# Kernel tuning notes

Measured on AMD Instinct MI355X. Metric: run time of the kernel, lower is better.

The kernel has to match this reference:

```python
import jax, jax.numpy as jnp
import numpy as np

MAX_DISP = 48
PATCH = 3
OFFSET = 0
PAD = PATCH // 2
EPS = 1e-3


def _unfold(x, P, pad):
    # x: [B,C,H,W] -> [B,C,K2,H,W], K2 enumerated row-major over the PxP window
    B, C, H, W = x.shape
    xp = jnp.pad(x, ((0, 0), (0, 0), (pad, pad), (pad, pad)))
    return jnp.stack([xp[:, :, i:i + H, j:j + W]
                      for i in range(P) for j in range(P)], axis=2)


def _normalize(x, axes):
    # torch F.normalize: x / clamp(||x||_2, min=eps)
    n = jnp.sqrt(jnp.sum(x * x, axis=axes, keepdims=True))
    return x / jnp.maximum(n, EPS)


def setup_inputs() -> dict:
    key = jax.random.key(0)
    k1, k2, k3 = jax.random.split(key, 3)
    shp = (2, 32, 128, 416)
    return {
        "xl": jax.random.normal(k1, shp, dtype=jnp.float32),
        "xm": jax.random.normal(k2, shp, dtype=jnp.float32),
        "xr": jax.random.normal(k3, shp, dtype=jnp.float32),
    }


def reference(xl, xm, xr):
    B, C, H, W = xl.shape
    K2 = PATCH * PATCH
    scale = (C * K2) ** 0.5

    pl = _normalize(_unfold(xl, PATCH, PAD), (1, 2))  # [B,C,K2,H,W]
    pr = _normalize(_unfold(xr, PATCH, PAD), (1, 2))
    fl = _normalize(xm, (1,))                          # [B,C,H,W]

    # fl is constant over the K2 axis, so sum patches over K2 once for sim_L/sim_R
    Sl = pl.sum(axis=2)  # [B,C,H,W]
    Sr = pr.sum(axis=2)

    cL, cR, cLR = [], [], []
    for d in range(OFFSET, OFFSET + MAX_DISP):
        if d > 0:
            # shifted_l[w] = patches_l[w+d] (zero right pad); shifted_r[w] = patches_r[w-d]
            sL = jnp.einsum('bchw,bchw->bhw', fl[..., :W - d], Sl[..., d:])
            sL = jnp.pad(sL, ((0, 0), (0, 0), (0, d)))
            sR = jnp.einsum('bchw,bchw->bhw', fl[..., d:], Sr[..., :W - d])
            sR = jnp.pad(sR, ((0, 0), (0, 0), (d, 0)))
            wlr = W - 2 * d  # overlap region of the two opposite shifts
            if wlr > 0:
                sLR = jnp.einsum('bckhw,bckhw->bhw', pl[..., 2 * d:], pr[..., :wlr])
                sLR = jnp.pad(sLR, ((0, 0), (0, 0), (d, d)))
            else:
                sLR = jnp.zeros((B, H, W), xl.dtype)
        else:
            sL = jnp.einsum('bchw,bchw->bhw', fl, Sl)
            sR = jnp.einsum('bchw,bchw->bhw', fl, Sr)
            sLR = jnp.einsum('bckhw,bckhw->bhw', pl, pr)
        cL.append(sL / scale)
        cR.append(sR / scale)
        cLR.append(sLR / scale)

    cost = jnp.stack([jnp.stack(cL, 1), jnp.stack(cR, 1), jnp.stack(cLR, 1)], axis=1)
    return jnp.clip(cost, -10.0, 10.0).astype(jnp.float16)  # [B,3,D,H,W]
```

## Files before the change

kernel.cpp:

```cpp
#include <hip/hip_runtime.h>
#include <math.h>

#define B 2
#define C 32
#define H 128
#define W 416
#define D 48
#define HW (H*W)
#define CHW (C*HW)
#define EPSN 1e-3f
#define ISCALE 0.05892556509887896f
#define ESTR 36
#define DSPL (D / 2)

typedef _Float16 h16;
typedef _Float16 __attribute__((ext_vector_type(2))) h16x2;

__device__ __forceinline__ float clip10(float x) {
    return fminf(fmaxf(x, -10.0f), 10.0f);
}

__device__ __forceinline__ float fdot2(h16x2 a, h16x2 bb, float c) {
    return __builtin_amdgcn_fdot2(a, bb, c, false);
}
__device__ __forceinline__ h16x2 u2h(unsigned int u) {
    union { unsigned int u; h16x2 h; } cv; cv.u = u; return cv.h;
}
__device__ __forceinline__ unsigned int pkh(float a, float bb) {
    union { h16x2 h; unsigned int u; } cv;
    cv.h = h16x2{(h16)a, (h16)bb}; return cv.u;
}

#define FMA4(acc, f, k, u) acc += f[4*(k)+0]*(u).x + f[4*(k)+1]*(u).y \
                               + f[4*(k)+2]*(u).z + f[4*(k)+3]*(u).w;

#define CLW(v) ((v) < 0 ? 0 : ((v) > (W - 1) ? (W - 1) : (v)))

__global__ __launch_bounds__(256) void k_norm(const float* __restrict__ sql,
                                              const float* __restrict__ sqr,
                                              float* __restrict__ inl,
                                              float* __restrict__ inr) {
    int idx = blockIdx.x * 256 + threadIdx.x;
    if (idx >= B * HW) return;
    int b = idx / HW, hw = idx - b * HW;
    int h = hw / W, w = hw - h * W;
    float sl = 0.f, sr = 0.f;
#pragma unroll
    for (int di = -1; di <= 1; ++di) {
        int hh = h + di;
        if (hh < 0 || hh >= H) continue;
#pragma unroll
        for (int dj = -1; dj <= 1; ++dj) {
            int ww = w + dj;
            if (ww < 0 || ww >= W) continue;
            int p = b * HW + hh * W + ww;
            sl += sql[p];
            sr += sqr[p];
        }
    }
    inl[idx] = 1.0f / fmaxf(sqrtf(sl), EPSN);
    inr[idx] = 1.0f / fmaxf(sqrtf(sr), EPSN);
}

__device__ __forceinline__ void stage_row_v2(const float* __restrict__ gsrc,
                                             float* __restrict__ lds,
                                             int tid, int nthreads) {
    for (int t = tid; t < (W / 4) * C; t += nthreads) {
        int rw = t & 7;
        int cl = (t >> 3) & 7;
        int g  = t >> 6;
        int wg = g % 13;
        int ch = g / 13;
        int c  = ch * 8 + cl;
        int w4 = (wg * 8 + rw) * 4;
        float4 v = *(const float4*)(gsrc + (size_t)c * HW + w4);
        lds[(w4 + 0) * ESTR + c] = v.x;
        lds[(w4 + 1) * ESTR + c] = v.y;
        lds[(w4 + 2) * ESTR + c] = v.z;
        lds[(w4 + 3) * ESTR + c] = v.w;
    }
}

__device__ __forceinline__ void stage_row3_h(const float* __restrict__ gsrc,
                                             unsigned int* __restrict__ lds,
                                             int h, int tid, int nthreads) {
    for (int t = tid; t < (W / 4) * (C / 2); t += nthreads) {
        int p = t & 15;
        int u = t >> 4;
        int v0 = 4 * u;
        const float* pa = gsrc + (size_t)(2 * p) * HW + v0;
        const float* pb = pa + HW;
        float4 va = *(const float4*)pa;
        float4 vb = *(const float4*)pb;
        if (h > 0) {
            float4 xa = *(const float4*)(pa - W);
            float4 xb = *(const float4*)(pb - W);
            va.x += xa.x; va.y += xa.y; va.z += xa.z; va.w += xa.w;
            vb.x += xb.x; vb.y += xb.y; vb.z += xb.z; vb.w += xb.w;
        }
        if (h < H - 1) {
            float4 xa = *(const float4*)(pa + W);
            float4 xb = *(const float4*)(pb + W);
            va.x += xa.x; va.y += xa.y; va.z += xa.z; va.w += xa.w;
            vb.x += xb.x; vb.y += xb.y; vb.z += xb.z; vb.w += xb.w;
        }
        int q = p >> 2, lo = p & 3;
        unsigned int pk0 = pkh(va.x, vb.x);
        unsigned int pk1 = pkh(va.y, vb.y);
        unsigned int pk2 = pkh(va.z, vb.z);
        unsigned int pk3 = pkh(va.w, vb.w);
#define PUTH(vv, val) { int _v = (vv); \
    lds[16 * (_v ^ ((_v >> 1) & 1)) \
        + 4 * (q ^ ((((_v) >> 1) ^ ((_v) >> 2)) & 3)) + lo] = (val); }
        PUTH(v0 + 0, pk0)
        PUTH(v0 + 1, pk1)
        PUTH(v0 + 2, pk2)
        PUTH(v0 + 3, pk3)
#undef PUTH
    }
}

__device__ __forceinline__ float dot32e(const float* __restrict__ x,
                                        const float* __restrict__ col) {
    const float4* c4 = (const float4*)col;
    float4 u0 = c4[0], u1 = c4[1], u2 = c4[2], u3 = c4[3];
    float4 u4 = c4[4], u5 = c4[5], u6 = c4[6], u7 = c4[7];
    float a = 0.f, bb = 0.f;
    FMA4(a, x, 0, u0) FMA4(a, x, 1, u1) FMA4(a, x, 2, u2) FMA4(a, x, 3, u3)
    FMA4(bb, x, 4, u4) FMA4(bb, x, 5, u5) FMA4(bb, x, 6, u6) FMA4(bb, x, 7, u7)
    return a + bb;
}

__global__ __launch_bounds__(512) void k_lr(const float* __restrict__ xm,
                                            const float* __restrict__ xl,
                                            const float* __restrict__ xr,
                                            const float* __restrict__ inl,
                                            const float* __restrict__ inr,
                                            float* __restrict__ out) {
    __shared__ unsigned int sBuL[W * 16];
    __shared__ unsigned int sBuR[W * 16];
    __shared__ float sInL[W];
    __shared__ float sInR[W];
    int tid = threadIdx.x;
    int grp = tid >> 8;
    int t8 = tid & 255;
    int h = blockIdx.x;
    int b = blockIdx.y;
    int d0 = blockIdx.z * DSPL;
    bool act = t8 < (W / 2);
    int w = 2 * t8;
    int bhw = b * HW + h * W;
    const float* pm = xm + (size_t)b * CHW + h * W;

    h16x2 f0h[16], f1h[16];
    if (act) {
        float t0[C], t1[C];
        float am0 = 0.f, am1 = 0.f;
#pragma unroll
        for (int c = 0; c < C; ++c) {
            float2 mv = *(const float2*)(pm + (size_t)c * HW + w);
            t0[c] = mv.x; t1[c] = mv.y;
            am0 += mv.x * mv.x; am1 += mv.y * mv.y;
        }
        float im0 = 1.0f / fmaxf(sqrtf(am0), EPSN);
        float im1 = 1.0f / fmaxf(sqrtf(am1), EPSN);
#pragma unroll
        for (int j = 0; j < 16; ++j) {
            f0h[j] = h16x2{(h16)(t0[2 * j] * im0), (h16)(t0[2 * j + 1] * im0)};
            f1h[j] = h16x2{(h16)(t1[2 * j] * im1), (h16)(t1[2 * j + 1] * im1)};
        }
    } else {
#pragma unroll
        for (int j = 0; j < 16; ++j) { f0h[j] = h16x2{(h16)0.f, (h16)0.f};
                                       f1h[j] = h16x2{(h16)0.f, (h16)0.f}; }
    }

    stage_row3_h(xl + (size_t)b * CHW + h * W, sBuL, h, tid, 512);
    stage_row3_h(xr + (size_t)b * CHW + h * W, sBuR, h, tid, 512);
    for (int j = tid; j < W; j += 512) {
        sInL[j] = inl[bhw + j];
        sInR[j] = inr[bhw + j];
    }
    __syncthreads();

    uint4 RA0, RA1, RA2, RA3;
    uint4 RB0, RB1, RB2, RB3;

#define LOADH(P, buf, vv) { int _v = CLW(vv); \
    const uint4* _c4 = (const uint4*)((buf) + 16 * (_v ^ ((_v >> 1) & 1))); \
    int _ky = ((_v >> 1) ^ (_v >> 2)) & 3; \
    P##0 = _c4[_ky]; P##1 = _c4[1 ^ _ky]; P##2 = _c4[2 ^ _ky]; P##3 = _c4[3 ^ _ky]; }

#define DOTH(P, c0, c1) { \
    float _a0 = 0.f, _a1 = 0.f, _b0 = 0.f, _b1 = 0.f; \
    _a0 = fdot2(f0h[0],  u2h((P##0).x), _a0); _a0 = fdot2(f0h[1],  u2h((P##0).y), _a0); \
    _a0 = fdot2(f0h[2],  u2h((P##0).z), _a0); _a0 = fdot2(f0h[3],  u2h((P##0).w), _a0); \
    _a0 = fdot2(f0h[4],  u2h((P##1).x), _a0); _a0 = fdot2(f0h[5],  u2h((P##1).y), _a0); \
    _a0 = fdot2(f0h[6],  u2h((P##1).z), _a0); _a0 = fdot2(f0h[7],  u2h((P##1).w), _a0); \
    _a1 = fdot2(f0h[8],  u2h((P##2).x), _a1); _a1 = fdot2(f0h[9],  u2h((P##2).y), _a1); \
    _a1 = fdot2(f0h[10], u2h((P##2).z), _a1); _a1 = fdot2(f0h[11], u2h((P##2).w), _a1); \
    _a1 = fdot2(f0h[12], u2h((P##3).x), _a1); _a1 = fdot2(f0h[13], u2h((P##3).y), _a1); \
    _a1 = fdot2(f0h[14], u2h((P##3).z), _a1); _a1 = fdot2(f0h[15], u2h((P##3).w), _a1); \
    _b0 = fdot2(f1h[0],  u2h((P##0).x), _b0); _b0 = fdot2(f1h[1],  u2h((P##0).y), _b0); \
    _b0 = fdot2(f1h[2],  u2h((P##0).z), _b0); _b0 = fdot2(f1h[3],  u2h((P##0).w), _b0); \
    _b0 = fdot2(f1h[4],  u2h((P##1).x), _b0); _b0 = fdot2(f1h[5],  u2h((P##1).y), _b0); \
    _b0 = fdot2(f1h[6],  u2h((P##1).z), _b0); _b0 = fdot2(f1h[7],  u2h((P##1).w), _b0); \
    _b1 = fdot2(f1h[8],  u2h((P##2).x), _b1); _b1 = fdot2(f1h[9],  u2h((P##2).y), _b1); \
    _b1 = fdot2(f1h[10], u2h((P##2).z), _b1); _b1 = fdot2(f1h[11], u2h((P##2).w), _b1); \
    _b1 = fdot2(f1h[12], u2h((P##3).x), _b1); _b1 = fdot2(f1h[13], u2h((P##3).y), _b1); \
    _b1 = fdot2(f1h[14], u2h((P##3).z), _b1); _b1 = fdot2(f1h[15], u2h((P##3).w), _b1); \
    c0 = _a0 + _a1; c1 = _b0 + _b1; }

    if (act && grp == 0) {
        float* oL = out + ((size_t)b * 3 + 0) * D * HW + h * W;
        const int vb = w + d0 - 1;
        float g0a = 0.f, g0b = 0.f, g1a = 0.f, g1b = 0.f, s0p = 0.f;
#define STEPL(P, jj) { int v = vb + (jj); bool ok = (v >= 0) && (v < W); \
    float c0, c1; DOTH(P, c0, c1); c0 = ok ? c0 : 0.f; c1 = ok ? c1 : 0.f; \
    float s0 = 0.f, s1 = 0.f; \
    if ((jj) >= 2) { int m = v - 1; \
        if (m < W) { float sc = sInL[m] * ISCALE; \
            s0 = clip10((g0a + g0b + c0) * sc); s1 = clip10((g1a + g1b + c1) * sc); } \
        if ((jj) >= 3) { int d = d0 + (jj) - 3; \
            *(float2*)(oL + (size_t)d * HW + w) = make_float2(s0p, s1); } } \
    s0p = s0; g0a = g0b; g0b = c0; g1a = g1b; g1b = c1; }
        LOADH(RA, sBuL, vb);
#pragma unroll 2
        for (int j = 0; j < DSPL + 2; j += 2) {
            LOADH(RB, sBuL, vb + j + 1);
            STEPL(RA, j);
            LOADH(RA, sBuL, vb + j + 2);
            STEPL(RB, j + 1);
        }
        STEPL(RA, DSPL + 2);
#undef STEPL
    } else if (act) {
        float* oR = out + ((size_t)b * 3 + 1) * D * HW + h * W;
        const int vb = w - d0 - DSPL;
        float g0a = 0.f, g0b = 0.f, g1a = 0.f, g1b = 0.f, s0p = 0.f;
#define STEPR(P, jj) { int v = vb + (jj); bool ok = (v >= 0) && (v < W); \
    float c0, c1; DOTH(P, c0, c1); c0 = ok ? c0 : 0.f; c1 = ok ? c1 : 0.f; \
    float s0 = 0.f, s1 = 0.f; \
    if ((jj) >= 2) { int m = v - 1; \
        if (m >= 0) { float sc = sInR[m] * ISCALE; \
            s0 = clip10((g0a + g0b + c0) * sc); s1 = clip10((g1a + g1b + c1) * sc); } \
        if ((jj) >= 3) { int d = d0 + DSPL + 2 - (jj); \
            *(float2*)(oR + (size_t)d * HW + w) = make_float2(s0p, s1); } } \
    s0p = s0; g0a = g0b; g0b = c0; g1a = g1b; g1b = c1; }
        LOADH(RA, sBuR, vb);
#pragma unroll 2
        for (int j = 0; j < DSPL + 2; j += 2) {
            LOADH(RB, sBuR, vb + j + 1);
            STEPR(RA, j);
            LOADH(RA, sBuR, vb + j + 2);
            STEPR(RB, j + 1);
        }
        STEPR(RA, DSPL + 2);
#undef STEPR
    }
#undef LOADH
#undef DOTH
}

__global__ __launch_bounds__(448, 4) void k_e(const float* __restrict__ xl,
                                              const float* __restrict__ xr,
                                              _Float16* __restrict__ EH,
                                              float* __restrict__ sql,
                                              float* __restrict__ sqr) {
    __shared__ float sXL[W * ESTR];
    int tid = threadIdx.x;
    int h = blockIdx.x;
    int b = blockIdx.y;
    int d0 = blockIdx.z * DSPL;
    int lane = tid & 63;
    int wv = tid >> 6;
    int v = wv * 62 + lane - 1;
    bool vin = (v >= 0) && (v < W);
    const float* br = xr + (size_t)b * CHW + h * W;

    float xrv[C];
#pragma unroll
    for (int c = 0; c < C; ++c) xrv[c] = vin ? br[c * HW + v] : 0.0f;

    stage_row_v2(xl + (size_t)b * CHW + h * W, sXL, tid, 448);
    __syncthreads();

    bool wr = (lane >= 1) && (lane <= 62) && (v < W);

    if (blockIdx.z == 0) {
        float sr_ = 0.f, sl_ = 0.f;
#pragma unroll
        for (int c = 0; c < C; ++c) sr_ += xrv[c] * xrv[c];
        if (vin) {
            const float4* c4 = (const float4*)(sXL + v * ESTR);
#pragma unroll
            for (int q = 0; q < 8; ++q) {
                float4 x = c4[q];
                sl_ += x.x * x.x + x.y * x.y + x.z * x.z + x.w * x.w;
            }
        }
        if (wr) {
            sqr[b * HW + h * W + v] = sr_;
            sql[b * HW + h * W + v] = sl_;
        }
    }

    _Float16* pe = EH + (((size_t)b * D) * H + h) * W + v;

    float4 RA0, RA1, RA2, RA3, RA4, RA5, RA6, RA7;
    float4 RB0, RB1, RB2, RB3, RB4, RB5, RB6, RB7;

#define LOADE(P, col) { int _vq = CLW(col); \
    const float4* _c4 = (const float4*)(sXL + (size_t)_vq * ESTR); \
    P##0 = _c4[0]; P##1 = _c4[1]; P##2 = _c4[2]; P##3 = _c4[3]; \
    P##4 = _c4[4]; P##5 = _c4[5]; P##6 = _c4[6]; P##7 = _c4[7]; }
#define STEPE(P, dd) { float _a = 0.f, _b = 0.f; \
    FMA4(_a, xrv, 0, P##0) FMA4(_a, xrv, 1, P##1) FMA4(_a, xrv, 2, P##2) FMA4(_a, xrv, 3, P##3) \
    FMA4(_b, xrv, 4, P##4) FMA4(_b, xrv, 5, P##5) FMA4(_b, xrv, 6, P##6) FMA4(_b, xrv, 7, P##7) \
    float e = (vin && (v + 2 * (dd)) < W) ? (_a + _b) : 0.f; \
    float em = __shfl_up(e, 1); \
    float ep = __shfl_down(e, 1); \
    float eh = em + e + ep; \
    if (wr) pe[(size_t)(dd) * HW] = (_Float16)eh; }

    LOADE(RA, v + 2 * d0);
#pragma unroll 2
    for (int d = d0; d < d0 + DSPL; d += 2) {
        LOADE(RB, v + 2 * d + 2);
        STEPE(RA, d);
        LOADE(RA, v + 2 * d + 4);
        STEPE(RB, d + 1);
    }
#undef LOADE
#undef STEPE
}

#define DCH 12
__global__ __launch_bounds__(448) void k_lr2(const _Float16* __restrict__ EH,
                                             const float* __restrict__ inl,
                                             const float* __restrict__ inr,
                                             float* __restrict__ out) {
    int w = threadIdx.x;
    int dc = blockIdx.x;
    int h = blockIdx.y;
    int b = blockIdx.z;
    if (w >= W) return;
    int bhw = b * HW + h * W;
    bool hm = (h > 0), hp = (h < H - 1);

    float* o = out + ((size_t)b * 3 + 2) * D * HW + h * W + w;
#pragma unroll
    for (int i = 0; i < DCH; ++i) {
        int d = dc * DCH + i;
        float r = 0.0f;
        if (w >= d && w + d < W) {
            int vc = w - d;
            const _Float16* base = EH + ((size_t)b * D + d) * HW + vc;
            float e = (float)base[h * W];
            if (hm) e += (float)base[(h - 1) * W];
            if (hp) e += (float)base[(h + 1) * W];
            float nl = inl[bhw + w + d];
            float nr = inr[bhw + vc];
            r = clip10(e * nl * nr * ISCALE);
        }
        o[(size_t)d * HW] = r;
    }
}

extern "C" void kernel_launch(void* const* d_in, const int* in_sizes, int n_in,
                              void* d_out, int out_size, void* d_ws, size_t ws_size,
                              hipStream_t stream) {
    const float* xl = (const float*)d_in[0];
    const float* xm = (const float*)d_in[1];
    const float* xr = (const float*)d_in[2];
    float* out = (float*)d_out;

    float* ws = (float*)d_ws;
    float* inl = ws;
    float* inr = inl + B * HW;
    float* sql = inr + B * HW;
    float* sqr = sql + B * HW;
    _Float16* EH = (_Float16*)(sqr + B * HW);

    k_e<<<dim3(H, B, 2), dim3(448), 0, stream>>>(xl, xr, EH, sql, sqr);
    k_norm<<<dim3((B * HW + 255) / 256), dim3(256), 0, stream>>>(sql, sqr, inl, inr);
    k_lr<<<dim3(H, B, 2), dim3(512), 0, stream>>>(xm, xl, xr, inl, inr, out);
    k_lr2<<<dim3(4, H, B), dim3(448), 0, stream>>>(EH, inl, inr, out);
}
```

Baseline: 161.9 us.

## Fuse LR cost-volume epilogue into k_lr as a third thread group

```diff
diff --git a/kernel.cpp b/kernel.cpp
--- a/kernel.cpp
+++ b/kernel.cpp
@@ -120,22 +120,12 @@
     }
 }
 
-__device__ __forceinline__ float dot32e(const float* __restrict__ x,
-                                        const float* __restrict__ col) {
-    const float4* c4 = (const float4*)col;
-    float4 u0 = c4[0], u1 = c4[1], u2 = c4[2], u3 = c4[3];
-    float4 u4 = c4[4], u5 = c4[5], u6 = c4[6], u7 = c4[7];
-    float a = 0.f, bb = 0.f;
-    FMA4(a, x, 0, u0) FMA4(a, x, 1, u1) FMA4(a, x, 2, u2) FMA4(a, x, 3, u3)
-    FMA4(bb, x, 4, u4) FMA4(bb, x, 5, u5) FMA4(bb, x, 6, u6) FMA4(bb, x, 7, u7)
-    return a + bb;
-}
-
-__global__ __launch_bounds__(512) void k_lr(const float* __restrict__ xm,
+__global__ __launch_bounds__(768) void k_lr(const float* __restrict__ xm,
                                             const float* __restrict__ xl,
                                             const float* __restrict__ xr,
                                             const float* __restrict__ inl,
                                             const float* __restrict__ inr,
+                                            const _Float16* __restrict__ EH,
                                             float* __restrict__ out) {
     __shared__ unsigned int sBuL[W * 16];
     __shared__ unsigned int sBuR[W * 16];
@@ -153,7 +143,7 @@
     const float* pm = xm + (size_t)b * CHW + h * W;
 
     h16x2 f0h[16], f1h[16];
-    if (act) {
+    if (act && grp < 2) {
         float t0[C], t1[C];
         float am0 = 0.f, am1 = 0.f;
 #pragma unroll
@@ -175,9 +165,9 @@
                                        f1h[j] = h16x2{(h16)0.f, (h16)0.f}; }
     }
 
-    stage_row3_h(xl + (size_t)b * CHW + h * W, sBuL, h, tid, 512);
-    stage_row3_h(xr + (size_t)b * CHW + h * W, sBuR, h, tid, 512);
-    for (int j = tid; j < W; j += 512) {
+    stage_row3_h(xl + (size_t)b * CHW + h * W, sBuL, h, tid, 768);
+    stage_row3_h(xr + (size_t)b * CHW + h * W, sBuR, h, tid, 768);
+    for (int j = tid; j < W; j += 768) {
         sInL[j] = inl[bhw + j];
         sInR[j] = inr[bhw + j];
     }
@@ -234,7 +224,7 @@
         }
         STEPL(RA, DSPL + 2);
 #undef STEPL
-    } else if (act) {
+    } else if (act && grp == 1) {
         float* oR = out + ((size_t)b * 3 + 1) * D * HW + h * W;
         const int vb = w - d0 - DSPL;
         float g0a = 0.f, g0b = 0.f, g1a = 0.f, g1b = 0.f, s0p = 0.f;
@@ -257,16 +247,41 @@
         }
         STEPR(RA, DSPL + 2);
 #undef STEPR
+    } else if (act) {
+        float* oC = out + ((size_t)b * 3 + 2) * D * HW + h * W;
+        bool hm = (h > 0), hp = (h < H - 1);
+#pragma unroll 4
+        for (int i = 0; i < DSPL; ++i) {
+            int d = d0 + i;
+            const _Float16* base = EH + ((size_t)b * D + d) * HW + h * W;
+            float r0 = 0.f, r1 = 0.f;
+            if (w >= d && w + d < W) {
+                int vc = w - d;
+                float e = (float)base[vc];
+                if (hm) e += (float)base[vc - W];
+                if (hp) e += (float)base[vc + W];
+                r0 = clip10(e * sInL[w + d] * sInR[vc] * ISCALE);
+            }
+            int w1 = w + 1;
+            if (w1 >= d && w1 + d < W) {
+                int vc = w1 - d;
+                float e = (float)base[vc];
+                if (hm) e += (float)base[vc - W];
+                if (hp) e += (float)base[vc + W];
+                r1 = clip10(e * sInL[w1 + d] * sInR[vc] * ISCALE);
+            }
+            *(float2*)(oC + (size_t)d * HW + w) = make_float2(r0, r1);
+        }
     }
 #undef LOADH
 #undef DOTH
 }
 
-__global__ __launch_bounds__(448, 4) void k_e(const float* __restrict__ xl,
-                                              const float* __restrict__ xr,
-                                              _Float16* __restrict__ EH,
-                                              float* __restrict__ sql,
-                                              float* __restrict__ sqr) {
+__global__ __launch_bounds__(448) void k_e(const float* __restrict__ xl,
+                                           const float* __restrict__ xr,
+                                           _Float16* __restrict__ EH,
+                                           float* __restrict__ sql,
+                                           float* __restrict__ sqr) {
     __shared__ float sXL[W * ESTR];
     int tid = threadIdx.x;
     int h = blockIdx.x;
@@ -335,38 +350,6 @@
 #undef STEPE
 }
 
-#define DCH 12
-__global__ __launch_bounds__(448) void k_lr2(const _Float16* __restrict__ EH,
-                                             const float* __restrict__ inl,
-                                             const float* __restrict__ inr,
-                                             float* __restrict__ out) {
-    int w = threadIdx.x;
-    int dc = blockIdx.x;
-    int h = blockIdx.y;
-    int b = blockIdx.z;
-    if (w >= W) return;
-    int bhw = b * HW + h * W;
-    bool hm = (h > 0), hp = (h < H - 1);
-
-    float* o = out + ((size_t)b * 3 + 2) * D * HW + h * W + w;
-#pragma unroll
-    for (int i = 0; i < DCH; ++i) {
-        int d = dc * DCH + i;
-        float r = 0.0f;
-        if (w >= d && w + d < W) {
-            int vc = w - d;
-            const _Float16* base = EH + ((size_t)b * D + d) * HW + vc;
-            float e = (float)base[h * W];
-            if (hm) e += (float)base[(h - 1) * W];
-            if (hp) e += (float)base[(h + 1) * W];
-            float nl = inl[bhw + w + d];
-            float nr = inr[bhw + vc];
-            r = clip10(e * nl * nr * ISCALE);
-        }
-        o[(size_t)d * HW] = r;
-    }
-}
-
 extern "C" void kernel_launch(void* const* d_in, const int* in_sizes, int n_in,
                               void* d_out, int out_size, void* d_ws, size_t ws_size,
                               hipStream_t stream) {
@@ -384,6 +367,5 @@
 
     k_e<<<dim3(H, B, 2), dim3(448), 0, stream>>>(xl, xr, EH, sql, sqr);
     k_norm<<<dim3((B * HW + 255) / 256), dim3(256), 0, stream>>>(sql, sqr, inl, inr);
-    k_lr<<<dim3(H, B, 2), dim3(512), 0, stream>>>(xm, xl, xr, inl, inr, out);
-    k_lr2<<<dim3(4, H, B), dim3(448), 0, stream>>>(EH, inl, inr, out);
-}
+    k_lr<<<dim3(H, B, 2), dim3(768), 0, stream>>>(xm, xl, xr, inl, inr, EH, out);
+}
```

After: 184.9 us. 1.14x slower.
